# Optimization experiments

Hardware: AMD Instinct MI355X
Metric: run time of the kernel (lower is better)

Reference implementation:

```python
import jax, jax.numpy as jnp
import numpy as np

NH, DK, DV, KC = 12, 64, 128, 4  # heads, head_qk_dim, head_v_dim, conv_size


def causal_dwconv(x, w):
    # x: [B, L, C], w: [C, K] depthwise causal conv (torch Conv1d groups=C with left pad K-1)
    K = w.shape[1]
    L = x.shape[1]
    xp = jnp.pad(x, ((0, 0), (K - 1, 0), (0, 0)))
    out = xp[:, 0:L, :] * w[:, 0]
    for j in range(1, K):
        out = out + xp[:, j:j + L, :] * w[:, j]
    return out


def l2norm(x, eps=1e-12):
    n = jnp.sqrt(jnp.sum(x * x, axis=-1, keepdims=True))
    return x / jnp.maximum(n, eps)


def rmsnorm(x, eps=1e-5):
    return x * jax.lax.rsqrt(jnp.mean(x * x, axis=-1, keepdims=True) + eps)


def setup_inputs() -> dict:
    key = jax.random.key(0)
    ks = jax.random.split(key, 16)
    B, L, H = 4, 2048, 1024
    Kd, Vd = 768, 1536  # key_dim, value_dim
    s = 0.02
    inp = {
        'hidden_states': jax.random.normal(ks[0], (B, L, H), jnp.float32),
        'Wq': jax.random.normal(ks[1], (H, Kd), jnp.float32) * s,
        'Wk': jax.random.normal(ks[2], (H, Kd), jnp.float32) * s,
        'Wv': jax.random.normal(ks[3], (H, Vd), jnp.float32) * s,
        'Wg': jax.random.normal(ks[4], (H, Vd), jnp.float32) * s,
        'Wgk': jax.random.normal(ks[5], (H, NH), jnp.float32) * s,
        'Wb': jax.random.normal(ks[6], (H, NH), jnp.float32) * s,
        'bb': jnp.zeros((NH,), jnp.float32),
        'conv_q': jax.random.normal(ks[7], (Kd, KC), jnp.float32) * 0.3,
        'conv_k': jax.random.normal(ks[8], (Kd, KC), jnp.float32) * 0.3,
        'conv_v': jax.random.normal(ks[9], (Vd, KC), jnp.float32) * 0.3,
        'A_log': jnp.log(jax.random.uniform(ks[10], (NH,), jnp.float32, 1e-4, 16.0)),
        'gnorm_w': jnp.ones((DV,), jnp.float32),
        'Wo': jax.random.normal(ks[11], (Vd, H), jnp.float32) * s,
    }
    dt = jnp.exp(jax.random.uniform(ks[12], (NH,), jnp.float32) * (np.log(0.1) - np.log(0.001)) + np.log(0.001))
    dt = jnp.clip(dt, 1e-4, None)
    inp['dt_bias'] = dt + jnp.log(-jnp.expm1(-dt))
    return inp


def reference(hidden_states, Wq, Wk, Wv, Wg, Wgk, Wb, bb, conv_q, conv_k, conv_v, A_log, dt_bias, gnorm_w, Wo):
    B, L, H = hidden_states.shape
    # projections + causal depthwise short conv with silu (qk_norm='l2')
    q = jax.nn.silu(causal_dwconv(hidden_states @ Wq, conv_q))
    k = jax.nn.silu(causal_dwconv(hidden_states @ Wk, conv_k))
    v = jax.nn.silu(causal_dwconv(hidden_states @ Wv, conv_v))
    # mamba-style decay gate: gk = -exp(A_log) * softplus(x Wgk + dt_bias)  -> [B,L,NH]
    gk = -jnp.exp(A_log) * jax.nn.softplus(hidden_states @ Wgk + dt_bias)
    beta = jax.nn.sigmoid(hidden_states @ Wb + bb)  # [B,L,NH]
    q = l2norm(q.reshape(B, L, NH, DK))
    k = l2norm(k.reshape(B, L, NH, DK))
    v = v.reshape(B, L, NH, DV)

    # gated delta rule recurrence: S_t = exp(gk_t) * S_{t-1}; S_t += k_t (beta_t (v_t - k_t^T S_t)); o_t = q_t^T S_t
    def step(S, inp_t):
        qt, kt, vt, gt, bt = inp_t
        S = S * jnp.exp(gt)[..., None, None]
        pred = jnp.einsum('bhk,bhkv->bhv', kt, S)
        delta = bt[..., None] * (vt - pred)
        S = S + kt[..., None] * delta[:, :, None, :]
        ot = jnp.einsum('bhk,bhkv->bhv', qt, S)
        return S, ot

    xs = (jnp.moveaxis(q, 1, 0), jnp.moveaxis(k, 1, 0), jnp.moveaxis(v, 1, 0),
          jnp.moveaxis(gk, 1, 0), jnp.moveaxis(beta, 1, 0))
    S0 = jnp.zeros((B, NH, DK, DV), hidden_states.dtype)
    _, o = jax.lax.scan(step, S0, xs)
    o = jnp.moveaxis(o, 0, 1)  # [B,L,NH,DV]

    # fused RMSNorm + swish gate, then output projection
    g = (hidden_states @ Wg).reshape(B, L, NH, DV)
    o = rmsnorm(o) * gnorm_w * jax.nn.silu(g)
    return o.reshape(B, L, NH * DV) @ Wo
```

## Files before the change

kernel.cpp:

```cpp
#include <hip/hip_runtime.h>

#define B_   4
#define L_   2048
#define H_   1024
#define KD   768
#define VD   1536
#define NHh  12
#define DKh  64
#define DVh  128
#define M_   (B_ * L_)
#define NC   32
#define NCID (B_ * NHh * NC)

using bf16x8 = __attribute__((ext_vector_type(8))) __bf16;
using f32x4  = __attribute__((ext_vector_type(4))) float;
using ui4    = __attribute__((ext_vector_type(4))) unsigned int;
using f4v    = __attribute__((ext_vector_type(4))) float;
using u16x4  = __attribute__((ext_vector_type(4))) unsigned short;
using u16x8  = __attribute__((ext_vector_type(8))) unsigned short;

__device__ __forceinline__ float bf2f(unsigned short u) {
  unsigned int x = ((unsigned int)u) << 16;
  return __builtin_bit_cast(float, x);
}
__device__ __forceinline__ unsigned short f2bf(float f) {
  unsigned int u = __builtin_bit_cast(unsigned int, f);
  u += 0x7fffu + ((u >> 16) & 1u);
  return (unsigned short)(u >> 16);
}
__device__ __forceinline__ float sigmoidf_(float x) { return 1.f / (1.f + __expf(-x)); }

__device__ __forceinline__ void async_copy16(const unsigned short* __restrict__ g,
                                             unsigned short* l) {
  __builtin_amdgcn_global_load_lds((const __attribute__((address_space(1))) unsigned int*)g,
                                   (__attribute__((address_space(3))) unsigned int*)l, 16, 0, 0);
}

__global__ void detect_dtype(const unsigned short* __restrict__ hs, int* __restrict__ flag) {
  int tid = threadIdx.x;
  int cnt = 0;
  for (int i = tid; i < 1024; i += 256) {
    int e = (hs[i] >> 7) & 0xFF;
    if (e >= 134) cnt++;
  }
  #pragma unroll
  for (int off = 32; off; off >>= 1) cnt += __shfl_xor(cnt, off);
  __shared__ int red[4];
  if ((tid & 63) == 0) red[tid >> 6] = cnt;
  __syncthreads();
  if (tid == 0) *flag = (red[0] + red[1] + red[2] + red[3] > 100) ? 1 : 0;
}

__global__ void convert_hs4(const void* __restrict__ src, unsigned short* __restrict__ dst,
                            const int* __restrict__ flag) {
  size_t i = ((size_t)blockIdx.x * 256 + threadIdx.x) * 4;
  if (*flag) {
    f4v v = *(const f4v*)((const float*)src + i);
    u16x4 o;
    o.x = f2bf(v[0]); o.y = f2bf(v[1]); o.z = f2bf(v[2]); o.w = f2bf(v[3]);
    *(u16x4*)(dst + i) = o;
  } else {
    *(u16x4*)(dst + i) = *(const u16x4*)((const unsigned short*)src + i);
  }
}

__global__ void convert_small(const void* s0, const void* s1, const void* s2,
                              const void* s3, const void* s4, const void* s5, const void* s6,
                              float* d0, float* d1, float* d2, float* d3, float* d4,
                              float* d5, float* d6, const int* __restrict__ flag) {
  const int sizes[7] = {KD * 4, KD * 4, VD * 4, NHh, NHh, NHh, DVh};
  int a = blockIdx.y;
  const void* s; float* d;
  switch (a) {
    case 0: s = s0; d = d0; break;  case 1: s = s1; d = d1; break;
    case 2: s = s2; d = d2; break;  case 3: s = s3; d = d3; break;
    case 4: s = s4; d = d4; break;  case 5: s = s5; d = d5; break;
    default: s = s6; d = d6; break;
  }
  int i = blockIdx.x * 256 + threadIdx.x;
  if (i >= sizes[a]) return;
  float v = (*flag) ? ((const float*)s)[i] : bf2f(((const unsigned short*)s)[i]);
  if (a < 3) {
    int C = (a == 2) ? VD : KD;
    d[(i & 3) * C + (i >> 2)] = v;
  } else {
    d[i] = v;
  }
}

__global__ void transpose_conv(const void* __restrict__ in, unsigned short* __restrict__ out,
                               int R, int C, const int* __restrict__ flag) {
  __shared__ unsigned short tile[32][33];
  int f = *flag;
  int c0 = blockIdx.x * 32, r0 = blockIdx.y * 32;
  int tx = threadIdx.x & 31, ty = threadIdx.x >> 5;
  #pragma unroll
  for (int i = 0; i < 32; i += 8) {
    int r = r0 + ty + i, c = c0 + tx;
    unsigned short v = 0;
    if (r < R && c < C)
      v = f ? f2bf(((const float*)in)[(size_t)r * C + c])
            : ((const unsigned short*)in)[(size_t)r * C + c];
    tile[ty + i][tx] = v;
  }
  __syncthreads();
  #pragma unroll
  for (int i = 0; i < 32; i += 8) {
    int c = c0 + ty + i, r = r0 + tx;
    if (c < C && r < R) out[(size_t)c * R + r] = tile[tx][ty + i];
  }
}

#define BMt 128
#define BNt 128
#define BKt 64

__global__ __launch_bounds__(256, 2) void gemm_bt(
    const unsigned short* __restrict__ Ag,
    const unsigned short* __restrict__ BTg,
    void* __restrict__ Cg,
    int M, int N, int K, int f32mode, const int* __restrict__ flag) {
  __shared__ __align__(16) unsigned short As[BMt * BKt];
  __shared__ __align__(16) unsigned short Bs[BNt * BKt];
  const int tid = threadIdx.x;
  const int wave = tid >> 6, lane = tid & 63;
  const int wr = wave >> 1, wc = wave & 1;
  const int lrow = lane & 15, lq = lane >> 4;
  const int row0 = blockIdx.x * BMt;
  const int col0 = blockIdx.y * BNt;
  f32x4 acc[4][4] = {};
  for (int k0 = 0; k0 < K; k0 += BKt) {
    #pragma unroll
    for (int i = 0; i < 4; i++) {
      int c = i * 256 + tid;
      int r = c >> 3, kk = (c & 7) << 3;
      int ldsbase = (i * 256 + wave * 64) * 8;
      async_copy16(&Ag[(size_t)(row0 + r) * K + k0 + kk], &As[ldsbase]);
      async_copy16(&BTg[(size_t)(col0 + r) * K + k0 + kk], &Bs[ldsbase]);
    }
    __syncthreads();
    #pragma unroll
    for (int ks = 0; ks < BKt; ks += 32) {
      bf16x8 af[4], bfr[4];
      #pragma unroll
      for (int i = 0; i < 4; i++) {
        af[i]  = *(const bf16x8*)&As[(wr * 64 + i * 16 + lrow) * BKt + ks + lq * 8];
        bfr[i] = *(const bf16x8*)&Bs[(wc * 64 + i * 16 + lrow) * BKt + ks + lq * 8];
      }
      #pragma unroll
      for (int mi = 0; mi < 4; mi++)
        #pragma unroll
        for (int ni = 0; ni < 4; ni++)
          acc[mi][ni] = __builtin_amdgcn_mfma_f32_16x16x32_bf16(af[mi], bfr[ni], acc[mi][ni], 0, 0, 0);
    }
    __syncthreads();
  }
  bool f32 = (f32mode == 1) || (f32mode == 2 && *flag != 0);
  #pragma unroll
  for (int mi = 0; mi < 4; mi++)
    #pragma unroll
    for (int ni = 0; ni < 4; ni++)
      #pragma unroll
      for (int r = 0; r < 4; r++) {
        size_t idx = (size_t)(row0 + wr * 64 + mi * 16 + lq * 4 + r) * N
                   + (col0 + wc * 64 + ni * 16 + lrow);
        float v = acc[mi][ni][r];
        if (f32) ((float*)Cg)[idx] = v;
        else     ((unsigned short*)Cg)[idx] = f2bf(v);
      }
}

__global__ void gkbeta_kernel(const float* __restrict__ logits,
                              const float* __restrict__ bb,
                              const float* __restrict__ A_log,
                              const float* __restrict__ dt_bias,
                              float* __restrict__ gkb, float* __restrict__ betab) {
  int idx = blockIdx.x * 256 + threadIdx.x;
  int m = idx / 24, j = idx - m * 24;
  float x = logits[(size_t)m * 128 + j];
  if (j < 12) {
    float t = x + dt_bias[j];
    float sp = (t > 20.f) ? t : log1pf(__expf(t));
    gkb[m * NHh + j] = -__expf(A_log[j]) * sp;
  } else {
    betab[m * NHh + (j - 12)] = sigmoidf_(x + bb[j - 12]);
  }
}

__global__ __launch_bounds__(192) void conv_qk_kernel(
    const unsigned short* __restrict__ raw, int rstride,
    const float* __restrict__ w,
    unsigned short* __restrict__ outp) {
  int tid = threadIdx.x;
  int rib = tid / 96, within = tid - rib * 96;
  int bl = blockIdx.x * 2 + rib;
  int c = within * 8;
  int l = bl & (L_ - 1);
  float acc[8] = {};
  #pragma unroll
  for (int j = 0; j < 4; j++) {
    int ll = l - 3 + j;
    if (ll >= 0) {
      u16x8 v = *(const u16x8*)&raw[(size_t)(bl - 3 + j) * rstride + c];
      f4v w0 = *(const f4v*)&w[j * KD + c];
      f4v w1 = *(const f4v*)&w[j * KD + c + 4];
      #pragma unroll
      for (int e = 0; e < 4; e++) acc[e] += bf2f(v[e]) * w0[e];
      #pragma unroll
      for (int e = 0; e < 4; e++) acc[4 + e] += bf2f(v[4 + e]) * w1[e];
    }
  }
  float x[8], ss = 0.f;
  #pragma unroll
  for (int e = 0; e < 8; e++) {
    float a = acc[e];
    x[e] = a * sigmoidf_(a);
    ss += x[e] * x[e];
  }
  #pragma unroll
  for (int off = 1; off <= 4; off <<= 1) ss += __shfl_xor(ss, off);
  float inv = 1.f / fmaxf(sqrtf(ss), 1e-12f);
  u16x8 o;
  #pragma unroll
  for (int e = 0; e < 8; e++) o[e] = f2bf(x[e] * inv);
  *(u16x8*)&outp[(size_t)bl * KD + c] = o;
}

__global__ void conv_v_kernel(const unsigned short* __restrict__ raw,
                              const float* __restrict__ w,
                              unsigned short* __restrict__ outp) {
  int idx = blockIdx.x * 256 + threadIdx.x;
  int bl = idx / 192;
  int c = (idx - bl * 192) * 8;
  int l = bl & (L_ - 1);
  float acc[8] = {};
  #pragma unroll
  for (int j = 0; j < 4; j++) {
    int ll = l - 3 + j;
    if (ll >= 0) {
      u16x8 v = *(const u16x8*)&raw[(size_t)(bl - 3 + j) * VD + c];
      f4v w0 = *(const f4v*)&w[j * VD + c];
      f4v w1 = *(const f4v*)&w[j * VD + c + 4];
      #pragma unroll
      for (int e = 0; e < 4; e++) acc[e] += bf2f(v[e]) * w0[e];
      #pragma unroll
      for (int e = 0; e < 4; e++) acc[4 + e] += bf2f(v[4 + e]) * w1[e];
    }
  }
  u16x8 o;
  #pragma unroll
  for (int e = 0; e < 8; e++) {
    float a = acc[e];
    o[e] = f2bf(a * sigmoidf_(a));
  }
  *(u16x8*)&outp[(size_t)bl * VD + c] = o;
}

__global__ __launch_bounds__(256) void phase1_kernel(
    const unsigned short* __restrict__ kb, const unsigned short* __restrict__ vb,
    const float* __restrict__ gkb, const float* __restrict__ betab,
    unsigned short* __restrict__ U0g, unsigned short* __restrict__ Wmg,
    float* __restrict__ Gamg) {
  int cid = blockIdx.x;
  int c = cid & (NC - 1), bh = cid >> 5;
  int h = bh % NHh, b = bh / NHh;
  int bl0 = b * L_ + (c << 6);
  __shared__ __align__(16) unsigned short K_lds[64][72];
  __shared__ __align__(16) unsigned short Ab[64][72];
  __shared__ __align__(16) unsigned short Tb[64][72];
  __shared__ __align__(16) unsigned short TbT[64][72];
  __shared__ __align__(16) unsigned short Qt[64][40];
  __shared__ __align__(16) unsigned short Mpad[16][40];
  __shared__ __align__(16) unsigned short RHSt[192][72];
  __shared__ float G_lds[64], beta_lds[64], besc_lds[64];
  int tid = threadIdx.x;
  int wave = tid >> 6, lane = tid & 63, lq = lane >> 4, lrow = lane & 15;
  {
    u16x4 z = {};
    unsigned short* tb = &Tb[0][0];  unsigned short* tt = &TbT[0][0];
    for (int i = tid * 4; i < 64 * 72; i += 1024) {
      *(u16x4*)&tb[i] = z;  *(u16x4*)&tt[i] = z;
    }
    unsigned short* qt = &Qt[0][0];
    for (int i = tid * 4; i < 64 * 40; i += 1024) *(u16x4*)&qt[i] = z;
    if (tid < 160) *(u16x4*)&(&Mpad[0][0])[tid * 4] = z;
  }
  {
    int j = tid >> 2, d0 = (tid & 3) << 4;
    const ui4* src = (const ui4*)&kb[(size_t)(bl0 + j) * KD + h * 64 + d0];
    *(ui4*)&K_lds[j][d0]     = src[0];
    *(ui4*)&K_lds[j][d0 + 8] = src[1];
  }
  if (tid < 64) {
    float g  = gkb[(size_t)(bl0 + tid) * NHh + h];
    float bt = betab[(size_t)(bl0 + tid) * NHh + h];
    #pragma unroll
    for (int off = 1; off < 64; off <<= 1) {
      int src = lane - off;
      float y = __shfl(g, src < 0 ? 0 : src);
      if (lane >= off) g += y;
    }
    G_lds[tid]    = g;
    beta_lds[tid] = bt;
    besc_lds[tid] = bt * __expf(g);
    Gamg[(size_t)cid * 64 + tid] = g;
  }
  __syncthreads();
  #pragma unroll
  for (int mt = 0; mt < 4; mt++) {
    f32x4 acc = {};
    #pragma unroll
    for (int ks = 0; ks < 2; ks++) {
      bf16x8 a  = *(const bf16x8*)&K_lds[wave * 16 + lrow][ks * 32 + lq * 8];
      bf16x8 b2 = *(const bf16x8*)&K_lds[mt * 16 + lrow][ks * 32 + lq * 8];
      acc = __builtin_amdgcn_mfma_f32_16x16x32_bf16(a, b2, acc, 0, 0, 0);
    }
    #pragma unroll
    for (int r = 0; r < 4; r++) {
      int j = wave * 16 + lq * 4 + r, m = mt * 16 + lrow;
      Ab[j][m] = (m < j) ? f2bf(beta_lds[j] * __expf(G_lds[j] - G_lds[m]) * acc[r])
                         : (unsigned short)0;
    }
  }
  __syncthreads();
  if (wave == 0) {
    int blk = lq, cc = lrow, base = blk * 16;
    float t[16];
    t[0] = (cc == 0) ? 1.f : 0.f;
    #pragma unroll
    for (int j = 1; j < 16; j++) {
      float s = 0.f;
      #pragma unroll
      for (int m = 0; m < j; m++)
        s += bf2f(Ab[base + j][base + m]) * t[m];
      t[j] = ((cc == j) ? 1.f : 0.f) - s;
    }
    #pragma unroll
    for (int j = 0; j < 16; j++) {
      unsigned short bv = f2bf(t[j]);
      Tb[base + j][base + cc]  = bv;
      TbT[base + cc][base + j] = bv;
    }
  } else {
    int r = tid - 64;
    if (r < 128) {
      const unsigned short* vp = &vb[(size_t)bl0 * VD + h * 128 + r];
      for (int j = 0; j < 64; j++)
        RHSt[r][j] = f2bf(beta_lds[j] * bf2f(vp[(size_t)j * VD]));
    } else {
      int d = r - 128;
      for (int j = 0; j < 64; j++)
        RHSt[r][j] = f2bf(besc_lds[j] * bf2f(K_lds[j][d]));
    }
  }
  __syncthreads();
  #pragma unroll
  for (int lvl = 1; lvl < 4; lvl++) {
    {
      int m = tid >> 4, k = tid & 15;
      Ab[lvl * 16 + m][lvl * 16 + k] = 0;
      Mpad[m][k] = Tb[lvl * 16 + m][lvl * 16 + k];
    }
    __syncthreads();
    f32x4 accP = {};
    #pragma unroll
    for (int ks2 = 0; ks2 < 2; ks2++) {
      bf16x8 a  = *(const bf16x8*)&Ab[lvl * 16 + lrow][ks2 * 32 + lq * 8];
      bf16x8 b2 = *(const bf16x8*)&TbT[wave * 16 + lrow][ks2 * 32 + lq * 8];
      accP = __builtin_amdgcn_mfma_f32_16x16x32_bf16(a, b2, accP, 0, 0, 0);
    }
    {
      int col = wave * 16 + lrow;
      u16x4 qp;
      #pragma unroll
      for (int r = 0; r < 4; r++) {
        int krow = lq * 4 + r;
        float e = (col == lvl * 16 + krow) ? 1.f : 0.f;
        ((unsigned short*)&qp)[r] = f2bf(e - accP[r]);
      }
      *(u16x4*)&Qt[col][lq * 4] = qp;
    }
    __syncthreads();
    {
      bf16x8 am = *(const bf16x8*)&Mpad[lrow][lq * 8];
      bf16x8 bq = *(const bf16x8*)&Qt[wave * 16 + lrow][lq * 8];
      f32x4 accR = {};
      accR = __builtin_amdgcn_mfma_f32_16x16x32_bf16(am, bq, accR, 0, 0, 0);
      #pragma unroll
      for (int r = 0; r < 4; r++) {
        int row = lvl * 16 + lq * 4 + r, col = wave * 16 + lrow;
        unsigned short bv = f2bf(accR[r]);
        Tb[row][col]  = bv;
        TbT[col][row] = bv;
      }
    }
    __syncthreads();
  }
  bf16x8 af0 = *(const bf16x8*)&Tb[wave * 16 + lrow][lq * 8];
  bf16x8 af1 = *(const bf16x8*)&Tb[wave * 16 + lrow][32 + lq * 8];
  #pragma unroll
  for (int nt = 0; nt < 12; nt++) {
    f32x4 acc = {};
    bf16x8 b0 = *(const bf16x8*)&RHSt[nt * 16 + lrow][lq * 8];
    bf16x8 b1 = *(const bf16x8*)&RHSt[nt * 16 + lrow][32 + lq * 8];
    acc = __builtin_amdgcn_mfma_f32_16x16x32_bf16(af0, b0, acc, 0, 0, 0);
    acc = __builtin_amdgcn_mfma_f32_16x16x32_bf16(af1, b1, acc, 0, 0, 0);
    #pragma unroll
    for (int r = 0; r < 4; r++) {
      int i = wave * 16 + lq * 4 + r;
      int col = nt * 16 + lrow;
      if (nt < 8) U0g[(size_t)cid * 8192 + i * 128 + col] = f2bf(acc[r]);
      else        Wmg[(size_t)cid * 4096 + i * 64 + (col - 128)] = f2bf(acc[r]);
    }
  }
}

__global__ __launch_bounds__(256) void phase2_kernel(
    const unsigned short* __restrict__ kb,
    const unsigned short* __restrict__ U0g, const unsigned short* __restrict__ Wmg,
    const float* __restrict__ Gamg, unsigned short* __restrict__ P0g) {
  int blk = blockIdx.x;
  int vc = blk & 3, bh = blk >> 2;
  int h = bh % NHh, b = bh / NHh;
  __shared__ __align__(16) unsigned short P_bf[32][72];
  __shared__ __align__(16) unsigned short Wm_lds[64][72];
  __shared__ __align__(16) unsigned short Ktmp[64][72];
  __shared__ __align__(16) unsigned short KpT_lds[64][72];
  __shared__ __align__(16) unsigned short U0_lds[64][40];
  __shared__ __align__(16) unsigned short UT_lds[32][72];
  __shared__ float G2[64];
  int tid = threadIdx.x;
  int wave = tid >> 6, lane = tid & 63, lq = lane >> 4, lrow = lane & 15;
  int vt = wave & 1, dbase = (wave >> 1) * 2;
  f32x4 P[2] = {};
  int pj = tid >> 2, px = (tid & 3) << 4;
  int pv = (tid & 3) << 3;
  ui4 pf_wm0, pf_wm1, pf_k0, pf_k1, pf_u0;
  float pf_g = 0.f;
  {
    size_t cid0 = (size_t)bh * NC;
    int bl0 = b * L_;
    pf_wm0 = *(const ui4*)&Wmg[cid0 * 4096 + pj * 64 + px];
    pf_wm1 = *(const ui4*)&Wmg[cid0 * 4096 + pj * 64 + px + 8];
    pf_k0  = *(const ui4*)&kb[(size_t)(bl0 + pj) * KD + h * 64 + px];
    pf_k1  = *(const ui4*)&kb[(size_t)(bl0 + pj) * KD + h * 64 + px + 8];
    pf_u0  = *(const ui4*)&U0g[cid0 * 8192 + pj * 128 + vc * 32 + pv];
    if (tid < 64) pf_g = Gamg[cid0 * 64 + tid];
  }
  for (int c = 0; c < NC; c++) {
    size_t cid = (size_t)bh * NC + c;
    #pragma unroll
    for (int di = 0; di < 2; di++)
      #pragma unroll
      for (int r = 0; r < 4; r++)
        P_bf[vt * 16 + lq * 4 + r][(dbase + di) * 16 + lrow] = f2bf(P[di][r]);
    *(ui4*)&Wm_lds[pj][px]     = pf_wm0;
    *(ui4*)&Wm_lds[pj][px + 8] = pf_wm1;
    *(ui4*)&Ktmp[pj][px]       = pf_k0;
    *(ui4*)&Ktmp[pj][px + 8]   = pf_k1;
    *(ui4*)&U0_lds[pj][pv]     = pf_u0;
    if (tid < 64) G2[tid] = pf_g;
    __syncthreads();
    float gend = __expf(G2[63]);
    {
      int v = tid >> 3, d8 = (tid & 7) << 3;
      *(ui4*)&P0g[cid * 8192 + (size_t)(vc * 32 + v) * 64 + d8] = *(const ui4*)&P_bf[v][d8];
    }
    if (c + 1 < NC) {
      size_t cid1 = cid + 1;
      int bl1 = b * L_ + ((c + 1) << 6);
      pf_wm0 = *(const ui4*)&Wmg[cid1 * 4096 + pj * 64 + px];
      pf_wm1 = *(const ui4*)&Wmg[cid1 * 4096 + pj * 64 + px + 8];
      pf_k0  = *(const ui4*)&kb[(size_t)(bl1 + pj) * KD + h * 64 + px];
      pf_k1  = *(const ui4*)&kb[(size_t)(bl1 + pj) * KD + h * 64 + px + 8];
      pf_u0  = *(const ui4*)&U0g[cid1 * 8192 + pj * 128 + vc * 32 + pv];
      if (tid < 64) pf_g = Gamg[cid1 * 64 + tid];
    }
    {
      int d = tid & 63, j0 = (tid >> 6) << 4;
      float Ge = G2[63];
      #pragma unroll
      for (int i = 0; i < 16; i++) {
        int j = j0 + i;
        KpT_lds[d][j] = f2bf(__expf(Ge - G2[j]) * bf2f(Ktmp[j][d]));
      }
    }
    #pragma unroll
    for (int vt2 = 0; vt2 < 2; vt2++) {
      f32x4 acc = {};
      #pragma unroll
      for (int ks2 = 0; ks2 < 2; ks2++) {
        bf16x8 a  = *(const bf16x8*)&Wm_lds[wave * 16 + lrow][ks2 * 32 + lq * 8];
        bf16x8 b2 = *(const bf16x8*)&P_bf[vt2 * 16 + lrow][ks2 * 32 + lq * 8];
        acc = __builtin_amdgcn_mfma_f32_16x16x32_bf16(a, b2, acc, 0, 0, 0);
      }
      u16x4 p;
      #pragma unroll
      for (int r = 0; r < 4; r++) {
        int j = wave * 16 + lq * 4 + r;
        ((unsigned short*)&p)[r] = f2bf(bf2f(U0_lds[j][vt2 * 16 + lrow]) - acc[r]);
      }
      *(u16x4*)&UT_lds[vt2 * 16 + lrow][wave * 16 + lq * 4] = p;
    }
    __syncthreads();
    #pragma unroll
    for (int di = 0; di < 2; di++) {
      f32x4 acc = P[di];
      #pragma unroll
      for (int r = 0; r < 4; r++) acc[r] *= gend;
      #pragma unroll
      for (int ks2 = 0; ks2 < 2; ks2++) {
        bf16x8 a  = *(const bf16x8*)&UT_lds[vt * 16 + lrow][ks2 * 32 + lq * 8];
        bf16x8 b2 = *(const bf16x8*)&KpT_lds[(dbase + di) * 16 + lrow][ks2 * 32 + lq * 8];
        acc = __builtin_amdgcn_mfma_f32_16x16x32_bf16(a, b2, acc, 0, 0, 0);
      }
      P[di] = acc;
    }
  }
}

__global__ __launch_bounds__(256) void phase3_kernel(
    const unsigned short* __restrict__ qb, const unsigned short* __restrict__ kb,
    const unsigned short* __restrict__ U0g, const unsigned short* __restrict__ Wmg,
    const unsigned short* __restrict__ P0g, const float* __restrict__ Gamg,
    unsigned short* __restrict__ o_raw) {
  int cid = blockIdx.x;
  int c = cid & (NC - 1), bh = cid >> 5;
  int h = bh % NHh, b = bh / NHh;
  int bl0 = b * L_ + (c << 6);
  __shared__ __align__(16) unsigned short Q_lds[64][72];
  __shared__ __align__(16) unsigned short K_lds[64][72];
  __shared__ __align__(16) unsigned short WM_lds[64][72];
  __shared__ __align__(16) unsigned short P0_lds[128][72];
  __shared__ __align__(16) unsigned short U0_lds[64][128];
  __shared__ __align__(16) unsigned short UT_lds[128][72];
  __shared__ float G_lds[64];
  int tid = threadIdx.x;
  int wave = tid >> 6, lane = tid & 63, lq = lane >> 4, lrow = lane & 15;
  {
    int j = tid >> 2, d0 = (tid & 3) << 4;
    const ui4* qs = (const ui4*)&qb[(size_t)(bl0 + j) * KD + h * 64 + d0];
    *(ui4*)&Q_lds[j][d0] = qs[0];  *(ui4*)&Q_lds[j][d0 + 8] = qs[1];
    const ui4* ks = (const ui4*)&kb[(size_t)(bl0 + j) * KD + h * 64 + d0];
    *(ui4*)&K_lds[j][d0] = ks[0];  *(ui4*)&K_lds[j][d0 + 8] = ks[1];
    const ui4* ws = (const ui4*)&Wmg[(size_t)cid * 4096 + j * 64 + d0];
    *(ui4*)&WM_lds[j][d0] = ws[0]; *(ui4*)&WM_lds[j][d0 + 8] = ws[1];
    int v = tid >> 1, e0 = (tid & 1) << 5;
    const ui4* ps = (const ui4*)&P0g[(size_t)cid * 8192 + v * 64 + e0];
    *(ui4*)&P0_lds[v][e0]      = ps[0]; *(ui4*)&P0_lds[v][e0 + 8]  = ps[1];
    *(ui4*)&P0_lds[v][e0 + 16] = ps[2]; *(ui4*)&P0_lds[v][e0 + 24] = ps[3];
    int e1 = tid * 32;
    const ui4* us = (const ui4*)&U0g[(size_t)cid * 8192 + e1];
    ui4* ud = (ui4*)&U0_lds[0][e1];
    ud[0] = us[0]; ud[1] = us[1]; ud[2] = us[2]; ud[3] = us[3];
    if (tid < 64) G_lds[tid] = Gamg[(size_t)cid * 64 + tid];
  }
  __syncthreads();
  #pragma unroll
  for (int nt = 0; nt < 8; nt++) {
    f32x4 acc = {};
    #pragma unroll
    for (int ks2 = 0; ks2 < 2; ks2++) {
      bf16x8 a  = *(const bf16x8*)&WM_lds[wave * 16 + lrow][ks2 * 32 + lq * 8];
      bf16x8 b2 = *(const bf16x8*)&P0_lds[nt * 16 + lrow][ks2 * 32 + lq * 8];
      acc = __builtin_amdgcn_mfma_f32_16x16x32_bf16(a, b2, acc, 0, 0, 0);
    }
    u16x4 p;
    #pragma unroll
    for (int r = 0; r < 4; r++) {
      int j = wave * 16 + lq * 4 + r;
      ((unsigned short*)&p)[r] = f2bf(bf2f(U0_lds[j][nt * 16 + lrow]) - acc[r]);
    }
    *(u16x4*)&UT_lds[nt * 16 + lrow][wave * 16 + lq * 4] = p;
  }
  __syncthreads();
  #pragma unroll
  for (int mt = 0; mt < 4; mt++) {
    f32x4 acc = {};
    #pragma unroll
    for (int ks2 = 0; ks2 < 2; ks2++) {
      bf16x8 a  = *(const bf16x8*)&Q_lds[wave * 16 + lrow][ks2 * 32 + lq * 8];
      bf16x8 b2 = *(const bf16x8*)&K_lds[mt * 16 + lrow][ks2 * 32 + lq * 8];
      acc = __builtin_amdgcn_mfma_f32_16x16x32_bf16(a, b2, acc, 0, 0, 0);
    }
    #pragma unroll
    for (int r = 0; r < 4; r++) {
      int i = wave * 16 + lq * 4 + r, j = mt * 16 + lrow;
      WM_lds[i][j] = (j <= i) ? f2bf(__expf(G_lds[i] - G_lds[j]) * acc[r]) : (unsigned short)0;
    }
  }
  __syncthreads();
  #pragma unroll
  for (int nt = 0; nt < 8; nt++) {
    f32x4 accO = {}, accS = {};
    #pragma unroll
    for (int ks2 = 0; ks2 < 2; ks2++) {
      bf16x8 aM = *(const bf16x8*)&WM_lds[wave * 16 + lrow][ks2 * 32 + lq * 8];
      bf16x8 bU = *(const bf16x8*)&UT_lds[nt * 16 + lrow][ks2 * 32 + lq * 8];
      accO = __builtin_amdgcn_mfma_f32_16x16x32_bf16(aM, bU, accO, 0, 0, 0);
      bf16x8 aQ = *(const bf16x8*)&Q_lds[wave * 16 + lrow][ks2 * 32 + lq * 8];
      bf16x8 bP = *(const bf16x8*)&P0_lds[nt * 16 + lrow][ks2 * 32 + lq * 8];
      accS = __builtin_amdgcn_mfma_f32_16x16x32_bf16(aQ, bP, accS, 0, 0, 0);
    }
    #pragma unroll
    for (int r = 0; r < 4; r++) {
      int i = wave * 16 + lq * 4 + r;
      float o = accO[r] + __expf(G_lds[i]) * accS[r];
      o_raw[(size_t)(bl0 + i) * VD + h * 128 + nt * 16 + lrow] = f2bf(o);
    }
  }
}

__global__ void norm_gate_kernel(unsigned short* __restrict__ o_raw,
                                 const unsigned short* __restrict__ g,
                                 const float* __restrict__ gnw) {
  int tid = threadIdx.x;
  int r = blockIdx.x * 16 + (tid >> 4);
  int v = (tid & 15) * 8;
  u16x8 xo = *(const u16x8*)&o_raw[(size_t)r * DVh + v];
  u16x8 xg = *(const u16x8*)&g[(size_t)r * DVh + v];
  float x[8], ss = 0.f;
  #pragma unroll
  for (int e = 0; e < 8; e++) {
    x[e] = bf2f(xo[e]);
    ss += x[e] * x[e];
  }
  #pragma unroll
  for (int off = 1; off <= 8; off <<= 1) ss += __shfl_xor(ss, off);
  float inv = rsqrtf(ss * (1.f / (float)DVh) + 1e-5f);
  f4v w0 = *(const f4v*)&gnw[v];
  f4v w1 = *(const f4v*)&gnw[v + 4];
  u16x8 o;
  #pragma unroll
  for (int e = 0; e < 8; e++) {
    float gv = bf2f(xg[e]);
    float wv = (e < 4) ? w0[e] : w1[e - 4];
    o[e] = f2bf(x[e] * inv * wv * (gv * sigmoidf_(gv)));
  }
  *(u16x8*)&o_raw[(size_t)r * DVh + v] = o;
}

extern "C" void kernel_launch(void* const* d_in, const int* in_sizes, int n_in,
                              void* d_out, int out_size, void* d_ws, size_t ws_size,
                              hipStream_t stream) {
  const void* hs      = d_in[0];
  const void* Wq      = d_in[1];
  const void* Wk      = d_in[2];
  const void* Wv      = d_in[3];
  const void* Wg      = d_in[4];
  const void* Wgk     = d_in[5];
  const void* Wb      = d_in[6];
  const void* bb      = d_in[7];
  const void* cq      = d_in[8];
  const void* ck      = d_in[9];
  const void* cv      = d_in[10];
  const void* A_log   = d_in[11];
  const void* gnorm_w = d_in[12];
  const void* Wo      = d_in[13];
  const void* dt_bias = d_in[14];

  char* wsB = (char*)d_ws;
  size_t off = 0;
  auto walloc = [&](size_t bytes) -> char* {
    char* p = wsB + off;
    off += (bytes + 1023) & ~(size_t)1023;
    return p;
  };
  int* flag = (int*)walloc(1024);
  unsigned short* WqT   = (unsigned short*)walloc((size_t)KD * H_ * 2);
  unsigned short* WkT   = (unsigned short*)walloc((size_t)KD * H_ * 2);
  unsigned short* WvT   = (unsigned short*)walloc((size_t)VD * H_ * 2);
  unsigned short* WgT   = (unsigned short*)walloc((size_t)VD * H_ * 2);
  unsigned short* WgkbT = (unsigned short*)walloc((size_t)128 * H_ * 2);
  unsigned short* WoT   = (unsigned short*)walloc((size_t)H_ * VD * 2);
  float* cqf   = (float*)walloc((size_t)KD * 4 * 4);
  float* ckf   = (float*)walloc((size_t)KD * 4 * 4);
  float* cvf   = (float*)walloc((size_t)VD * 4 * 4);
  float* bbf   = (float*)walloc(NHh * 4);
  float* A_logf= (float*)walloc(NHh * 4);
  float* dtf   = (float*)walloc(NHh * 4);
  float* gnwf  = (float*)walloc(DVh * 4);
  float* gkb   = (float*)walloc((size_t)M_ * NHh * 4);
  float* betab = (float*)walloc((size_t)M_ * NHh * 4);
  float* Gamg  = (float*)walloc((size_t)NCID * 64 * 4);
  unsigned short* c_hs  = (unsigned short*)walloc((size_t)M_ * H_ * 2);
  unsigned short* qkraw = (unsigned short*)walloc((size_t)M_ * 1536 * 2);
  unsigned short* vraw  = (unsigned short*)walloc((size_t)M_ * VD * 2);
  unsigned short* gbuf  = (unsigned short*)walloc((size_t)M_ * VD * 2);
  unsigned short* qb    = (unsigned short*)walloc((size_t)M_ * KD * 2);
  unsigned short* kb    = (unsigned short*)walloc((size_t)M_ * KD * 2);
  unsigned short* vb    = (unsigned short*)walloc((size_t)M_ * VD * 2);
  float*          logits32 = (float*)vraw;
  unsigned short* Wmg   = c_hs;
  unsigned short* U0g   = qkraw;
  unsigned short* o_raw = vraw;
  unsigned short* P0g   = vb;

  detect_dtype<<<1, 256, 0, stream>>>((const unsigned short*)hs, flag);
  convert_small<<<dim3(24, 7), 256, 0, stream>>>(cq, ck, cv, bb, A_log, dt_bias, gnorm_w,
                                                 cqf, ckf, cvf, bbf, A_logf, dtf, gnwf, flag);
  transpose_conv<<<dim3(KD / 32, H_ / 32), 256, 0, stream>>>(Wq, WqT, H_, KD, flag);
  transpose_conv<<<dim3(KD / 32, H_ / 32), 256, 0, stream>>>(Wk, WkT, H_, KD, flag);
  transpose_conv<<<dim3(VD / 32, H_ / 32), 256, 0, stream>>>(Wv, WvT, H_, VD, flag);
  transpose_conv<<<dim3(VD / 32, H_ / 32), 256, 0, stream>>>(Wg, WgT, H_, VD, flag);
  transpose_conv<<<dim3(1, H_ / 32), 256, 0, stream>>>(Wgk, WgkbT, H_, NHh, flag);
  transpose_conv<<<dim3(1, H_ / 32), 256, 0, stream>>>(Wb, WgkbT + 12 * H_, H_, NHh, flag);
  transpose_conv<<<dim3(H_ / 32, VD / 32), 256, 0, stream>>>(Wo, WoT, VD, H_, flag);
  convert_hs4<<<(M_ * H_) / 1024, 256, 0, stream>>>(hs, c_hs, flag);

  gemm_bt<<<dim3(M_ / 128, 1536 / 128), 256, 0, stream>>>(c_hs, WqT, qkraw, M_, 1536, H_, 0, flag);
  gemm_bt<<<dim3(M_ / 128, 1), 256, 0, stream>>>(c_hs, WgkbT, logits32, M_, 128, H_, 1, flag);
  gkbeta_kernel<<<(M_ * 24) / 256, 256, 0, stream>>>(logits32, bbf, A_logf, dtf, gkb, betab);
  gemm_bt<<<dim3(M_ / 128, VD / 128), 256, 0, stream>>>(c_hs, WvT, vraw, M_, VD, H_, 0, flag);
  gemm_bt<<<dim3(M_ / 128, VD / 128), 256, 0, stream>>>(c_hs, WgT, gbuf, M_, VD, H_, 0, flag);

  conv_qk_kernel<<<M_ / 2, 192, 0, stream>>>(qkraw, 1536, cqf, qb);
  conv_qk_kernel<<<M_ / 2, 192, 0, stream>>>(qkraw + KD, 1536, ckf, kb);
  conv_v_kernel<<<(M_ * 192) / 256, 256, 0, stream>>>(vraw, cvf, vb);

  phase1_kernel<<<NCID, 256, 0, stream>>>(kb, vb, gkb, betab, U0g, Wmg, Gamg);
  phase2_kernel<<<B_ * NHh * 4, 256, 0, stream>>>(kb, U0g, Wmg, Gamg, P0g);
  phase3_kernel<<<NCID, 256, 0, stream>>>(qb, kb, U0g, Wmg, P0g, Gamg, o_raw);

  norm_gate_kernel<<<(M_ * NHh) / 16, 256, 0, stream>>>(o_raw, gbuf, gnwf);

  gemm_bt<<<dim3(M_ / 128, H_ / 128), 256, 0, stream>>>(o_raw, WoT, d_out, M_, H_, VD, 2, flag);
}
```

Baseline: 478.3 us.

## Double-buffer and swizzle GEMM LDS tiles, merge QK/V/G projections into one launch

The bf16 GEMM now uses two LDS buffers so the next K tile is copied asynchronously while MFMAs run on the current one. Tile columns are XOR-swizzled by row to avoid LDS bank conflicts on the fragment reads. A new output mode routes column blocks into three separate 1536-wide destination regions, which lets the Q/K, V and G projections run as a single launch. This relies on the transposed weights and output buffers sitting contiguously in memory. It also doubles the LDS used per block, which may limit how many blocks fit on a CU.

Measured after the change: 456.2 us. 1.05x faster.

```diff
diff --git a/kernel.cpp b/kernel.cpp
--- a/kernel.cpp
+++ b/kernel.cpp
@@ -120,32 +120,50 @@
     const unsigned short* __restrict__ BTg,
     void* __restrict__ Cg,
     int M, int N, int K, int f32mode, const int* __restrict__ flag) {
-  __shared__ __align__(16) unsigned short As[BMt * BKt];
-  __shared__ __align__(16) unsigned short Bs[BNt * BKt];
+  __shared__ __align__(16) unsigned short As[2][BMt * BKt];
+  __shared__ __align__(16) unsigned short Bs[2][BNt * BKt];
   const int tid = threadIdx.x;
   const int wave = tid >> 6, lane = tid & 63;
   const int wr = wave >> 1, wc = wave & 1;
   const int lrow = lane & 15, lq = lane >> 4;
   const int row0 = blockIdx.x * BMt;
-  const int col0 = blockIdx.y * BNt;
+  const int bcol0 = blockIdx.y * BNt;
+  unsigned short* Cb = (unsigned short*)Cg;
+  int col0 = bcol0, Nst = N;
+  if (f32mode == 3) {
+    int region = bcol0 / 1536;
+    Cb += (size_t)region * (size_t)M_ * 1536;
+    col0 = bcol0 - region * 1536;
+    Nst = 1536;
+  }
   f32x4 acc[4][4] = {};
-  for (int k0 = 0; k0 < K; k0 += BKt) {
+  auto stage = [&](int sb, int k0) {
     #pragma unroll
     for (int i = 0; i < 4; i++) {
       int c = i * 256 + tid;
-      int r = c >> 3, kk = (c & 7) << 3;
+      int r = c >> 3;
+      int kk = ((c & 7) ^ (r & 7)) << 3;
       int ldsbase = (i * 256 + wave * 64) * 8;
-      async_copy16(&Ag[(size_t)(row0 + r) * K + k0 + kk], &As[ldsbase]);
-      async_copy16(&BTg[(size_t)(col0 + r) * K + k0 + kk], &Bs[ldsbase]);
-    }
-    __syncthreads();
+      async_copy16(&Ag[(size_t)(row0 + r) * K + k0 + kk], &As[sb][ldsbase]);
+      async_copy16(&BTg[(size_t)(bcol0 + r) * K + k0 + kk], &Bs[sb][ldsbase]);
+    }
+  };
+  stage(0, 0);
+  __syncthreads();
+  int cur = 0;
+  for (int k0 = 0; k0 < K; k0 += BKt) {
+    if (k0 + BKt < K) stage(cur ^ 1, k0 + BKt);
     #pragma unroll
     for (int ks = 0; ks < BKt; ks += 32) {
       bf16x8 af[4], bfr[4];
       #pragma unroll
       for (int i = 0; i < 4; i++) {
-        af[i]  = *(const bf16x8*)&As[(wr * 64 + i * 16 + lrow) * BKt + ks + lq * 8];
-        bfr[i] = *(const bf16x8*)&Bs[(wc * 64 + i * 16 + lrow) * BKt + ks + lq * 8];
+        int ra = wr * 64 + i * 16 + lrow;
+        int sa = ((ks >> 3) + lq) ^ (ra & 7);
+        af[i]  = *(const bf16x8*)&As[cur][ra * BKt + (sa << 3)];
+        int rb = wc * 64 + i * 16 + lrow;
+        int sb2 = ((ks >> 3) + lq) ^ (rb & 7);
+        bfr[i] = *(const bf16x8*)&Bs[cur][rb * BKt + (sb2 << 3)];
       }
       #pragma unroll
       for (int mi = 0; mi < 4; mi++)
@@ -154,6 +172,7 @@
           acc[mi][ni] = __builtin_amdgcn_mfma_f32_16x16x32_bf16(af[mi], bfr[ni], acc[mi][ni], 0, 0, 0);
     }
     __syncthreads();
+    cur ^= 1;
   }
   bool f32 = (f32mode == 1) || (f32mode == 2 && *flag != 0);
   #pragma unroll
@@ -162,11 +181,11 @@
     for (int ni = 0; ni < 4; ni++)
       #pragma unroll
       for (int r = 0; r < 4; r++) {
-        size_t idx = (size_t)(row0 + wr * 64 + mi * 16 + lq * 4 + r) * N
-                   + (col0 + wc * 64 + ni * 16 + lrow);
+        int rr = row0 + wr * 64 + mi * 16 + lq * 4 + r;
+        int cc = col0 + wc * 64 + ni * 16 + lrow;
         float v = acc[mi][ni][r];
-        if (f32) ((float*)Cg)[idx] = v;
-        else     ((unsigned short*)Cg)[idx] = f2bf(v);
+        if (f32) ((float*)Cg)[(size_t)rr * N + cc] = v;
+        else     Cb[(size_t)rr * Nst + cc] = f2bf(v);
       }
 }
 
@@ -708,11 +727,9 @@
   transpose_conv<<<dim3(H_ / 32, VD / 32), 256, 0, stream>>>(Wo, WoT, VD, H_, flag);
   convert_hs4<<<(M_ * H_) / 1024, 256, 0, stream>>>(hs, c_hs, flag);
 
-  gemm_bt<<<dim3(M_ / 128, 1536 / 128), 256, 0, stream>>>(c_hs, WqT, qkraw, M_, 1536, H_, 0, flag);
   gemm_bt<<<dim3(M_ / 128, 1), 256, 0, stream>>>(c_hs, WgkbT, logits32, M_, 128, H_, 1, flag);
   gkbeta_kernel<<<(M_ * 24) / 256, 256, 0, stream>>>(logits32, bbf, A_logf, dtf, gkb, betab);
-  gemm_bt<<<dim3(M_ / 128, VD / 128), 256, 0, stream>>>(c_hs, WvT, vraw, M_, VD, H_, 0, flag);
-  gemm_bt<<<dim3(M_ / 128, VD / 128), 256, 0, stream>>>(c_hs, WgT, gbuf, M_, VD, H_, 0, flag);
+  gemm_bt<<<dim3(M_ / 128, 4608 / 128), 256, 0, stream>>>(c_hs, WqT, qkraw, M_, 4608, H_, 3, flag);
 
   conv_qk_kernel<<<M_ / 2, 192, 0, stream>>>(qkraw, 1536, cqf, qb);
   conv_qk_kernel<<<M_ / 2, 192, 0, stream>>>(qkraw + KD, 1536, ckf, kb);
```
